# Kernel optimization log

Hardware: AMD Instinct MI355X
Metric: run time of the kernel (lower is better)

## Reference

```python
import jax, jax.numpy as jnp
import numpy as np

N_NODES = 50000
N_EDGES = 800000
N_IN = 96
N_HID = 96
N_CLS = 16
P_DROP = 0.5


def setup_inputs() -> dict:
    key = jax.random.key(0)
    ks = jax.random.split(key, 10)
    return {
        "features": jax.random.normal(ks[0], (N_NODES, N_IN), dtype=jnp.float32),
        "edge_weight": jax.random.uniform(ks[1], (N_EDGES,), dtype=jnp.float32),
        "src": jax.random.randint(ks[2], (N_EDGES,), 0, N_NODES),
        "dst": jax.random.randint(ks[3], (N_EDGES,), 0, N_NODES),
        "W0": jax.random.normal(ks[4], (N_IN, N_HID), dtype=jnp.float32) / np.sqrt(N_IN).astype(np.float32),
        "b0": jnp.zeros((N_HID,), dtype=jnp.float32),
        "W1": jax.random.normal(ks[5], (N_HID, N_HID), dtype=jnp.float32) / np.sqrt(N_HID).astype(np.float32),
        "b1": jnp.zeros((N_HID,), dtype=jnp.float32),
        "W2": jax.random.normal(ks[6], (N_HID, N_CLS), dtype=jnp.float32) / np.sqrt(N_HID).astype(np.float32),
        "b2": jnp.zeros((N_CLS,), dtype=jnp.float32),
    }


def reference(features, edge_weight, src, dst, W0, b0, W1, b1, W2, b2):
    N = features.shape[0]
    # Unweighted node degrees (DGL GraphConv norm='both'), clamped to >= 1.
    ones_e = jnp.ones_like(edge_weight)
    out_deg = jnp.clip(jax.ops.segment_sum(ones_e, src, num_segments=N), 1.0)
    in_deg = jnp.clip(jax.ops.segment_sum(ones_e, dst, num_segments=N), 1.0)
    inv_sqrt_out = out_deg ** -0.5  # [N]
    inv_sqrt_in = in_deg ** -0.5    # [N]

    def graph_conv(h, W, b, act):
        h = h * inv_sqrt_out[:, None]
        m = h[src] * edge_weight[:, None]                   # [E, d] gather + edge scale
        agg = jax.ops.segment_sum(m, dst, num_segments=N)   # [N, d] scatter-add
        out = (agg * inv_sqrt_in[:, None]) @ W + b          # D_in^-1/2, then linear + bias
        return act(out) if act is not None else out

    layers = [(W0, b0, jax.nn.relu), (W1, b1, jax.nn.relu), (W2, b2, None)]
    dkey = jax.random.key(42)
    h = features
    for i, (W, b, act) in enumerate(layers):
        keep = jax.random.bernoulli(jax.random.fold_in(dkey, i), 1.0 - P_DROP, h.shape)
        h = jnp.where(keep, h / (1.0 - P_DROP), 0.0)        # dropout p=0.5
        h = graph_conv(h, W, b, act)
    return jax.nn.log_softmax(h, axis=1)
```

## Files before the change

### kernel.cpp

```cpp
#include <hip/hip_runtime.h>
#include <hip/hip_fp16.h>
#include <stdint.h>

#define NNODES 50000
#define NEDGES 800000
#define NHID 96
#define NCLS 16

#define NC 100
#define NR 4
#define EPB (NEDGES / NC)
#define RNODES (NNODES / NR)
#define RWORDS8 (RNODES / 4)
#define NWORDS8 (NNODES / 4)
#define SCANB ((NWORDS8 + 255) / 256)
#define HISTBLKS (NC * NR)
#define FEPT8 8
#define FILLB3 ((NEDGES / FEPT8 + 255) / 256)
#define G96B ((NNODES + 127) / 128)
#define NDROP4 ((NNODES * NHID / 4 + 255) / 256)

__host__ __device__ inline void tf2x32(uint32_t k0, uint32_t k1, uint32_t x0, uint32_t x1,
                                       uint32_t& o0, uint32_t& o1) {
  uint32_t k2 = k0 ^ k1 ^ 0x1BD11BDAu;
#define TFROT(v, r) (((v) << (r)) | ((v) >> (32 - (r))))
#define TFR(r) { x0 += x1; x1 = TFROT(x1, r); x1 ^= x0; }
  x0 += k0; x1 += k1;
  TFR(13) TFR(15) TFR(26) TFR(6)
  x0 += k1; x1 += k2 + 1u;
  TFR(17) TFR(29) TFR(16) TFR(24)
  x0 += k2; x1 += k0 + 2u;
  TFR(13) TFR(15) TFR(26) TFR(6)
  x0 += k0; x1 += k1 + 3u;
  TFR(17) TFR(29) TFR(16) TFR(24)
  x0 += k1; x1 += k2 + 4u;
  TFR(13) TFR(15) TFR(26) TFR(6)
  x0 += k2; x1 += k0 + 5u;
  o0 = x0; o1 = x1;
#undef TFR
#undef TFROT
}

__device__ inline bool keep_bit(uint32_t k0, uint32_t k1, uint32_t j) {
  uint32_t o0, o1;
  tf2x32(k0, k1, 0u, j, o0, o1);
  return (((o0 ^ o1) >> 31) == 0u);
}

__global__ __launch_bounds__(256) void hist_drop_kernel(
    const int* __restrict__ src, const int* __restrict__ dst,
    uint32_t* __restrict__ slabD, uint32_t* __restrict__ slabS,
    uint8_t* __restrict__ rank8, uint32_t* __restrict__ flags,
    const float* __restrict__ h, float* __restrict__ X,
    uint32_t k0, uint32_t k1) {
  __shared__ uint32_t HD[RWORDS8];
  __shared__ uint32_t HS[RWORDS8];
  const int tid = threadIdx.x, b = blockIdx.x;
  if (b >= HISTBLKS) {
    int j = ((b - HISTBLKS) * 256 + tid) * 4;
    if (j < NNODES * NHID) {
      float4 hv = *(const float4*)(h + j);
      float4 o;
      o.x = keep_bit(k0, k1, (uint32_t)(j + 0)) ? hv.x * 2.0f : 0.0f;
      o.y = keep_bit(k0, k1, (uint32_t)(j + 1)) ? hv.y * 2.0f : 0.0f;
      o.z = keep_bit(k0, k1, (uint32_t)(j + 2)) ? hv.z * 2.0f : 0.0f;
      o.w = keep_bit(k0, k1, (uint32_t)(j + 3)) ? hv.w * 2.0f : 0.0f;
      *(float4*)(X + j) = o;
    }
    return;
  }
  if (b == 0 && tid < SCANB) flags[tid] = 0;
  const int c = b / NR, r = b - c * NR;
  const int e0 = c * EPB, e1 = e0 + EPB;
  const int nbase = r * RNODES;
  for (int w = tid; w < RWORDS8; w += 256) { HD[w] = 0; HS[w] = 0; }
  __syncthreads();
  int e = e0 + tid;
  for (; e + 768 < e1; e += 1024) {
    int d0 = dst[e] - nbase,       d1 = dst[e + 256] - nbase;
    int d2 = dst[e + 512] - nbase, d3 = dst[e + 768] - nbase;
    int s0 = src[e] - nbase,       s1 = src[e + 256] - nbase;
    int s2 = src[e + 512] - nbase, s3 = src[e + 768] - nbase;
    if ((unsigned)d0 < (unsigned)RNODES) {
      int sh = (d0 & 3) * 8;
      uint32_t old = atomicAdd(&HD[d0 >> 2], 1u << sh);
      rank8[e] = (uint8_t)((old >> sh) & 0xFFu);
    }
    if ((unsigned)d1 < (unsigned)RNODES) {
      int sh = (d1 & 3) * 8;
      uint32_t old = atomicAdd(&HD[d1 >> 2], 1u << sh);
      rank8[e + 256] = (uint8_t)((old >> sh) & 0xFFu);
    }
    if ((unsigned)d2 < (unsigned)RNODES) {
      int sh = (d2 & 3) * 8;
      uint32_t old = atomicAdd(&HD[d2 >> 2], 1u << sh);
      rank8[e + 512] = (uint8_t)((old >> sh) & 0xFFu);
    }
    if ((unsigned)d3 < (unsigned)RNODES) {
      int sh = (d3 & 3) * 8;
      uint32_t old = atomicAdd(&HD[d3 >> 2], 1u << sh);
      rank8[e + 768] = (uint8_t)((old >> sh) & 0xFFu);
    }
    if ((unsigned)s0 < (unsigned)RNODES) atomicAdd(&HS[s0 >> 2], 1u << ((s0 & 3) * 8));
    if ((unsigned)s1 < (unsigned)RNODES) atomicAdd(&HS[s1 >> 2], 1u << ((s1 & 3) * 8));
    if ((unsigned)s2 < (unsigned)RNODES) atomicAdd(&HS[s2 >> 2], 1u << ((s2 & 3) * 8));
    if ((unsigned)s3 < (unsigned)RNODES) atomicAdd(&HS[s3 >> 2], 1u << ((s3 & 3) * 8));
  }
  for (; e < e1; e += 256) {
    int d = dst[e] - nbase;
    if ((unsigned)d < (unsigned)RNODES) {
      int sh = (d & 3) * 8;
      uint32_t old = atomicAdd(&HD[d >> 2], 1u << sh);
      rank8[e] = (uint8_t)((old >> sh) & 0xFFu);
    }
    int s = src[e] - nbase;
    if ((unsigned)s < (unsigned)RNODES) atomicAdd(&HS[s >> 2], 1u << ((s & 3) * 8));
  }
  __syncthreads();
  uint32_t* dpD = slabD + (size_t)b * RWORDS8;
  uint32_t* dpS = slabS + (size_t)b * RWORDS8;
  for (int w = tid; w < RWORDS8; w += 256) { dpD[w] = HD[w]; dpS[w] = HS[w]; }
}

__global__ __launch_bounds__(256) void reduce_scan_kernel(
    const uint32_t* __restrict__ slabD, const uint32_t* __restrict__ slabS,
    float* __restrict__ inv_o, float* __restrict__ inv_i,
    uint32_t* __restrict__ rel8, int* __restrict__ row_ptr,
    uint32_t* __restrict__ flags) {
  __shared__ int lds[256];
  __shared__ int base_s;
  const int tid = threadIdx.x, b = blockIdx.x;
  const int gw = b * 256 + tid;
  uint32_t runD = 0, runS = 0;
  int n0 = 0;
  if (gw < NWORDS8) {
    int r = gw / RWORDS8, lw = gw - r * RWORDS8;
    n0 = r * RNODES + 4 * lw;
#pragma unroll 4
    for (int c = 0; c < NC; ++c) {
      rel8[(size_t)c * NWORDS8 + gw] = runD;
      runD += slabD[(size_t)(c * NR + r) * RWORDS8 + lw];
      runS += slabS[(size_t)(c * NR + r) * RWORDS8 + lw];
    }
  }
  const int d0 = runD & 0xFF, d1 = (runD >> 8) & 0xFF,
            d2 = (runD >> 16) & 0xFF, d3 = runD >> 24;
  const int tsum = d0 + d1 + d2 + d3;
  lds[tid] = tsum;
  __syncthreads();
  for (int off = 1; off < 256; off <<= 1) {
    int t = (tid >= off) ? lds[tid - off] : 0;
    __syncthreads();
    lds[tid] += t;
    __syncthreads();
  }
  const int incl = lds[tid];
  if (tid == 255) atomicExch(&flags[b], 0x80000000u | (uint32_t)lds[255]);
  if (tid < 64) {
    uint32_t part = 0;
    if (tid < b) {
      uint32_t v;
      do { v = atomicAdd(&flags[tid], 0u); } while (!(v & 0x80000000u));
      part = v & 0x7FFFFFFFu;
    }
#pragma unroll
    for (int off = 32; off > 0; off >>= 1)
      part += __shfl_down((unsigned)part, off, 64);
    if (tid == 0) base_s = (int)part;
  }
  __syncthreads();
  const int base = base_s;
  if (gw < NWORDS8) {
    int excl = base + incl - tsum;
    *(int4*)(row_ptr + n0) = make_int4(excl, excl + d0, excl + d0 + d1, excl + d0 + d1 + d2);
    *(float4*)(inv_i + n0) = make_float4(
        rsqrtf(fmaxf((float)d0, 1.0f)), rsqrtf(fmaxf((float)d1, 1.0f)),
        rsqrtf(fmaxf((float)d2, 1.0f)), rsqrtf(fmaxf((float)d3, 1.0f)));
    int o0 = runS & 0xFF, o1 = (runS >> 8) & 0xFF, o2 = (runS >> 16) & 0xFF, o3 = runS >> 24;
    *(float4*)(inv_o + n0) = make_float4(
        rsqrtf(fmaxf((float)o0, 1.0f)), rsqrtf(fmaxf((float)o1, 1.0f)),
        rsqrtf(fmaxf((float)o2, 1.0f)), rsqrtf(fmaxf((float)o3, 1.0f)));
    if (gw == NWORDS8 - 1) row_ptr[NNODES] = NEDGES;
  }
}

__global__ __launch_bounds__(256) void fill_gemm_kernel(
    const int* __restrict__ src, const int* __restrict__ dst, const float* __restrict__ ew,
    const uint8_t* __restrict__ rank8, const uint32_t* __restrict__ rel8,
    const int* __restrict__ row_ptr, const float* __restrict__ inv_o,
    uint32_t* __restrict__ csr,
    const float* __restrict__ X, const float* __restrict__ W, __half* __restrict__ Yh) {
  __shared__ float Wl[96 * 96];
  const int tid = threadIdx.x, b = blockIdx.x;
  if (b >= G96B) {
    int t = (b - G96B) * 256 + tid;
    int e = t * 8;
    if (e >= NEDGES) return;
    const uint32_t* rel = rel8 + (size_t)(e / EPB) * NWORDS8;
    int4 dA = *(const int4*)(dst + e), dB = *(const int4*)(dst + e + 4);
    int4 sA = *(const int4*)(src + e), sB = *(const int4*)(src + e + 4);
    float4 wA = *(const float4*)(ew + e), wB = *(const float4*)(ew + e + 4);
    uint2 r8 = *(const uint2*)(rank8 + e);
#pragma unroll
    for (int k = 0; k < 8; ++k) {
      int d = (k < 4) ? (&dA.x)[k] : (&dB.x)[k - 4];
      int s = (k < 4) ? (&sA.x)[k] : (&sB.x)[k - 4];
      float w = ((k < 4) ? (&wA.x)[k] : (&wB.x)[k - 4]) * inv_o[s];
      int rk = (int)(((k < 4 ? r8.x : r8.y) >> ((k & 3) * 8)) & 0xFFu);
      int sh = (d & 3) * 8;
      int rel_v = (int)((rel[d >> 2] >> sh) & 0xFFu);
      int pos = row_ptr[d] + rel_v + rk;
      uint32_t v = ((uint32_t)s << 16) | (uint32_t)__half_as_ushort(__float2half_rn(w));
      if ((unsigned)pos < (unsigned)NEDGES) csr[pos] = v;
    }
    return;
  }
  const int gb = b;
  {
    const float4* Wg = (const float4*)W;
    float4* Ws = (float4*)Wl;
#pragma unroll
    for (int i = 0; i < 9; ++i)
      Ws[tid + i * 256] = Wg[tid + i * 256];
  }
  __syncthreads();

  const int cg = tid & 7;
  const int rq = tid >> 3;
  const int row0 = gb * 128 + rq * 4;
  const int c0 = cg * 12;

  float acc[4][12];
#pragma unroll
  for (int r = 0; r < 4; ++r)
#pragma unroll
    for (int c = 0; c < 12; ++c) acc[r][c] = 0.f;

  const float* xr[4];
#pragma unroll
  for (int r = 0; r < 4; ++r) {
    int rr = row0 + r; if (rr > NNODES - 1) rr = NNODES - 1;
    xr[r] = X + (size_t)rr * 96;
  }

  for (int k = 0; k < 96; k += 4) {
    float4 x4[4];
#pragma unroll
    for (int r = 0; r < 4; ++r) x4[r] = *(const float4*)(xr[r] + k);
#pragma unroll
    for (int kk = 0; kk < 4; ++kk) {
      const float4* wp = (const float4*)(Wl + (k + kk) * 96 + c0);
      float4 w0 = wp[0], w1 = wp[1], w2 = wp[2];
      float xv[4] = { (&x4[0].x)[kk], (&x4[1].x)[kk], (&x4[2].x)[kk], (&x4[3].x)[kk] };
#pragma unroll
      for (int r = 0; r < 4; ++r) {
        acc[r][0]  += xv[r] * w0.x; acc[r][1]  += xv[r] * w0.y;
        acc[r][2]  += xv[r] * w0.z; acc[r][3]  += xv[r] * w0.w;
        acc[r][4]  += xv[r] * w1.x; acc[r][5]  += xv[r] * w1.y;
        acc[r][6]  += xv[r] * w1.z; acc[r][7]  += xv[r] * w1.w;
        acc[r][8]  += xv[r] * w2.x; acc[r][9]  += xv[r] * w2.y;
        acc[r][10] += xv[r] * w2.z; acc[r][11] += xv[r] * w2.w;
      }
    }
  }

#pragma unroll
  for (int r = 0; r < 4; ++r) {
    int rr = row0 + r;
    if (rr < NNODES) {
      __half2* hp = (__half2*)(Yh + (size_t)rr * 96 + c0);
#pragma unroll
      for (int c = 0; c < 6; ++c)
        hp[c] = __floats2half2_rn(acc[r][2 * c], acc[r][2 * c + 1]);
    }
  }
}

__global__ __launch_bounds__(256) void gemm96_kernel(
    const float* __restrict__ X, const float* __restrict__ W, __half* __restrict__ Yh) {
  __shared__ float Wl[96 * 96];
  const int tid = threadIdx.x;
  {
    const float4* Wg = (const float4*)W;
    float4* Ws = (float4*)Wl;
#pragma unroll
    for (int i = 0; i < 9; ++i)
      Ws[tid + i * 256] = Wg[tid + i * 256];
  }
  __syncthreads();

  const int cg = tid & 7;
  const int rq = tid >> 3;
  const int row0 = blockIdx.x * 128 + rq * 4;
  const int c0 = cg * 12;

  float acc[4][12];
#pragma unroll
  for (int r = 0; r < 4; ++r)
#pragma unroll
    for (int c = 0; c < 12; ++c) acc[r][c] = 0.f;

  const float* xr[4];
#pragma unroll
  for (int r = 0; r < 4; ++r) {
    int rr = row0 + r; if (rr > NNODES - 1) rr = NNODES - 1;
    xr[r] = X + (size_t)rr * 96;
  }

  for (int k = 0; k < 96; k += 4) {
    float4 x4[4];
#pragma unroll
    for (int r = 0; r < 4; ++r) x4[r] = *(const float4*)(xr[r] + k);
#pragma unroll
    for (int kk = 0; kk < 4; ++kk) {
      const float4* wp = (const float4*)(Wl + (k + kk) * 96 + c0);
      float4 w0 = wp[0], w1 = wp[1], w2 = wp[2];
      float xv[4] = { (&x4[0].x)[kk], (&x4[1].x)[kk], (&x4[2].x)[kk], (&x4[3].x)[kk] };
#pragma unroll
      for (int r = 0; r < 4; ++r) {
        acc[r][0]  += xv[r] * w0.x; acc[r][1]  += xv[r] * w0.y;
        acc[r][2]  += xv[r] * w0.z; acc[r][3]  += xv[r] * w0.w;
        acc[r][4]  += xv[r] * w1.x; acc[r][5]  += xv[r] * w1.y;
        acc[r][6]  += xv[r] * w1.z; acc[r][7]  += xv[r] * w1.w;
        acc[r][8]  += xv[r] * w2.x; acc[r][9]  += xv[r] * w2.y;
        acc[r][10] += xv[r] * w2.z; acc[r][11] += xv[r] * w2.w;
      }
    }
  }

#pragma unroll
  for (int r = 0; r < 4; ++r) {
    int rr = row0 + r;
    if (rr < NNODES) {
      __half2* hp = (__half2*)(Yh + (size_t)rr * 96 + c0);
#pragma unroll
      for (int c = 0; c < 6; ++c)
        hp[c] = __floats2half2_rn(acc[r][2 * c], acc[r][2 * c + 1]);
    }
  }
}

__global__ __launch_bounds__(256) void gemm16_kernel(
    const float* __restrict__ X, const float* __restrict__ W, __half* __restrict__ Y2h) {
  __shared__ float Wl[96 * 16];
  const int tid = threadIdx.x;
  {
    const float4* Wg = (const float4*)W;
    float4* Ws = (float4*)Wl;
    for (int i = tid; i < 384; i += 256) Ws[i] = Wg[i];
  }
  __syncthreads();

  const int row0 = blockIdx.x * 512 + tid * 2;
  const float* xr[2];
#pragma unroll
  for (int r = 0; r < 2; ++r) {
    int rr = row0 + r; if (rr > NNODES - 1) rr = NNODES - 1;
    xr[r] = X + (size_t)rr * 96;
  }

  float acc[2][16];
#pragma unroll
  for (int r = 0; r < 2; ++r)
#pragma unroll
    for (int c = 0; c < 16; ++c) acc[r][c] = 0.f;

  for (int k = 0; k < 96; k += 4) {
    float4 x4[2];
#pragma unroll
    for (int r = 0; r < 2; ++r) x4[r] = *(const float4*)(xr[r] + k);
#pragma unroll
    for (int kk = 0; kk < 4; ++kk) {
      const float4* wp = (const float4*)(Wl + (k + kk) * 16);
      float4 w0 = wp[0], w1 = wp[1], w2 = wp[2], w3 = wp[3];
#pragma unroll
      for (int r = 0; r < 2; ++r) {
        float xv = (&x4[r].x)[kk];
        acc[r][0]  += xv * w0.x; acc[r][1]  += xv * w0.y;
        acc[r][2]  += xv * w0.z; acc[r][3]  += xv * w0.w;
        acc[r][4]  += xv * w1.x; acc[r][5]  += xv * w1.y;
        acc[r][6]  += xv * w1.z; acc[r][7]  += xv * w1.w;
        acc[r][8]  += xv * w2.x; acc[r][9]  += xv * w2.y;
        acc[r][10] += xv * w2.z; acc[r][11] += xv * w2.w;
        acc[r][12] += xv * w3.x; acc[r][13] += xv * w3.y;
        acc[r][14] += xv * w3.z; acc[r][15] += xv * w3.w;
      }
    }
  }

#pragma unroll
  for (int r = 0; r < 2; ++r) {
    int rr = row0 + r;
    if (rr < NNODES) {
      __half2* hp = (__half2*)(Y2h + (size_t)rr * 16);
#pragma unroll
      for (int c = 0; c < 8; ++c)
        hp[c] = __floats2half2_rn(acc[r][2 * c], acc[r][2 * c + 1]);
    }
  }
}

#define ACC4(u0, wt) { \
  float2 g0 = __half22float2(*(__half2*)&u0.x); \
  float2 g1 = __half22float2(*(__half2*)&u0.y); \
  acc[0] += g0.x * wt; acc[1] += g0.y * wt; \
  acc[2] += g1.x * wt; acc[3] += g1.y * wt; }

__global__ __launch_bounds__(256) void gather96_drop_kernel(
    const __half* __restrict__ Yh, const uint32_t* __restrict__ csr,
    const int* __restrict__ row_ptr, const float* __restrict__ inv_in,
    const float* __restrict__ bias,
    float* __restrict__ Xn, uint32_t k0, uint32_t k1) {
  int tid = blockIdx.x * 256 + threadIdx.x;
  int n = tid / 24;
  int q = tid - n * 24;
  if (n >= NNODES) return;
  int beg = row_ptr[n], end = row_ptr[n + 1];
  float acc[4];
#pragma unroll
  for (int i = 0; i < 4; ++i) acc[i] = 0.f;

  int p = beg;
  for (; p + 8 <= end; p += 8) {
    uint32_t pw[8];
#pragma unroll
    for (int i = 0; i < 8; ++i) pw[i] = csr[p + i];
    float wv[8];
    uint2 u[8];
#pragma unroll
    for (int i = 0; i < 8; ++i) {
      int s = (int)(pw[i] >> 16); if (s >= NNODES) s = 0;
      wv[i] = __half2float(__ushort_as_half((unsigned short)(pw[i] & 0xFFFFu)));
      u[i] = *(const uint2*)(Yh + (size_t)s * 96 + q * 4);
    }
#pragma unroll
    for (int i = 0; i < 8; ++i) { ACC4(u[i], wv[i]) }
  }
  for (; p + 2 <= end; p += 2) {
    uint32_t pa = csr[p], pb = csr[p + 1];
    int s0 = pa >> 16, s1 = pb >> 16;
    if (s0 >= NNODES) s0 = 0;
    if (s1 >= NNODES) s1 = 0;
    float w0 = __half2float(__ushort_as_half((unsigned short)(pa & 0xFFFFu)));
    float w1 = __half2float(__ushort_as_half((unsigned short)(pb & 0xFFFFu)));
    uint2 a0 = *(const uint2*)(Yh + (size_t)s0 * 96 + q * 4);
    uint2 b0 = *(const uint2*)(Yh + (size_t)s1 * 96 + q * 4);
    ACC4(a0, w0)
    ACC4(b0, w1)
  }
  if (p < end) {
    uint32_t pa = csr[p];
    int s0 = pa >> 16;
    if (s0 >= NNODES) s0 = 0;
    float w0 = __half2float(__ushort_as_half((unsigned short)(pa & 0xFFFFu)));
    uint2 a0 = *(const uint2*)(Yh + (size_t)s0 * 96 + q * 4);
    ACC4(a0, w0)
  }

  float iv = inv_in[n];
  const float* bp = bias + q * 4;
  float o[4];
#pragma unroll
  for (int i = 0; i < 4; ++i)
    o[i] = fmaxf(acc[i] * iv + bp[i], 0.f) * 2.0f;
  uint32_t jb = (uint32_t)(n * 96 + q * 4);
#pragma unroll
  for (int i = 0; i < 4; ++i)
    o[i] = keep_bit(k0, k1, jb + i) ? o[i] : 0.f;
  float* xp = Xn + (size_t)n * 96 + q * 4;
  *(float4*)xp = make_float4(o[0], o[1], o[2], o[3]);
}

__global__ __launch_bounds__(256) void gather16_lsm_kernel(
    const __half* __restrict__ Y2h, const uint32_t* __restrict__ csr,
    const int* __restrict__ row_ptr, const float* __restrict__ inv_in,
    const float* __restrict__ b2, float* __restrict__ out) {
  int t = blockIdx.x * 256 + threadIdx.x;
  int n = t >> 2;
  int q = t & 3;
  if (n >= NNODES) return;
  int beg = row_ptr[n], end = row_ptr[n + 1];
  float acc[4];
#pragma unroll
  for (int i = 0; i < 4; ++i) acc[i] = 0.f;

  int p = beg;
  for (; p + 4 <= end; p += 4) {
    uint32_t pa = csr[p], pb = csr[p + 1], pc = csr[p + 2], pd = csr[p + 3];
    int sa = pa >> 16, sb = pb >> 16, sc_ = pc >> 16, sd = pd >> 16;
    if (sa >= NNODES) sa = 0;
    if (sb >= NNODES) sb = 0;
    if (sc_ >= NNODES) sc_ = 0;
    if (sd >= NNODES) sd = 0;
    float wa = __half2float(__ushort_as_half((unsigned short)(pa & 0xFFFFu)));
    float wb = __half2float(__ushort_as_half((unsigned short)(pb & 0xFFFFu)));
    float wc = __half2float(__ushort_as_half((unsigned short)(pc & 0xFFFFu)));
    float wd = __half2float(__ushort_as_half((unsigned short)(pd & 0xFFFFu)));
    uint2 a0 = *(const uint2*)(Y2h + (size_t)sa * 16 + q * 4);
    uint2 b0 = *(const uint2*)(Y2h + (size_t)sb * 16 + q * 4);
    uint2 c0 = *(const uint2*)(Y2h + (size_t)sc_ * 16 + q * 4);
    uint2 d0 = *(const uint2*)(Y2h + (size_t)sd * 16 + q * 4);
    ACC4(a0, wa) ACC4(b0, wb) ACC4(c0, wc) ACC4(d0, wd)
  }
  for (; p + 2 <= end; p += 2) {
    uint32_t pa = csr[p], pb = csr[p + 1];
    int sa = pa >> 16, sb = pb >> 16;
    if (sa >= NNODES) sa = 0;
    if (sb >= NNODES) sb = 0;
    float wa = __half2float(__ushort_as_half((unsigned short)(pa & 0xFFFFu)));
    float wb = __half2float(__ushort_as_half((unsigned short)(pb & 0xFFFFu)));
    uint2 a0 = *(const uint2*)(Y2h + (size_t)sa * 16 + q * 4);
    uint2 b0 = *(const uint2*)(Y2h + (size_t)sb * 16 + q * 4);
    ACC4(a0, wa) ACC4(b0, wb)
  }
  if (p < end) {
    uint32_t pa = csr[p];
    int sa = pa >> 16;
    if (sa >= NNODES) sa = 0;
    float wa = __half2float(__ushort_as_half((unsigned short)(pa & 0xFFFFu)));
    uint2 a0 = *(const uint2*)(Y2h + (size_t)sa * 16 + q * 4);
    ACC4(a0, wa)
  }

  float iv = inv_in[n];
  float v[4];
#pragma unroll
  for (int i = 0; i < 4; ++i) v[i] = acc[i] * iv + b2[q * 4 + i];
  float m = v[0];
#pragma unroll
  for (int i = 1; i < 4; i++) m = fmaxf(m, v[i]);
  m = fmaxf(m, __shfl_xor(m, 1));
  m = fmaxf(m, __shfl_xor(m, 2));
  float s = 0.f;
#pragma unroll
  for (int i = 0; i < 4; i++) s += expf(v[i] - m);
  s += __shfl_xor(s, 1);
  s += __shfl_xor(s, 2);
  float ls = logf(s);
  float* orow = out + (size_t)n * 16 + q * 4;
  *(float4*)orow = make_float4(v[0] - m - ls, v[1] - m - ls, v[2] - m - ls, v[3] - m - ls);
}

extern "C" void kernel_launch(void* const* d_in, const int* in_sizes, int n_in,
                              void* d_out, int out_size, void* d_ws, size_t ws_size,
                              hipStream_t stream) {
  const float* feat = (const float*)d_in[0];
  const float* ew   = (const float*)d_in[1];
  const int*   src  = (const int*)d_in[2];
  const int*   dst  = (const int*)d_in[3];
  const float* W0   = (const float*)d_in[4];
  const float* b0   = (const float*)d_in[5];
  const float* W1   = (const float*)d_in[6];
  const float* b1   = (const float*)d_in[7];
  const float* W2   = (const float*)d_in[8];
  const float* b2   = (const float*)d_in[9];
  float* out = (float*)d_out;

  char* base = (char*)d_ws;
  size_t off = 0;
  auto take = [&](size_t nbytes) {
    void* q = base + off;
    off += (nbytes + 255) & ~(size_t)255;
    return q;
  };
  uint32_t* flags   = (uint32_t*)take((size_t)SCANB * 4);
  int*      row_ptr = (int*)take((size_t)(NNODES + 1) * 4);
  float*    inv_o   = (float*)take((size_t)NNODES * 4);
  float*    inv_i   = (float*)take((size_t)NNODES * 4);
  uint32_t* slabD   = (uint32_t*)take((size_t)NC * NR * RWORDS8 * 4);
  uint32_t* slabS   = (uint32_t*)take((size_t)NC * NR * RWORDS8 * 4);
  uint32_t* rel8    = (uint32_t*)take((size_t)NC * NWORDS8 * 4);
  uint8_t*  rank8   = (uint8_t*)take((size_t)NEDGES);
  uint32_t* csr     = (uint32_t*)take((size_t)NEDGES * 4);
  float*    X       = (float*)take((size_t)NNODES * NHID * 4);
  __half*   Yh      = (__half*)take((size_t)NNODES * NHID * 2);
  __half*   Y2h     = (__half*)take((size_t)NNODES * NCLS * 2);
  (void)ws_size; (void)in_sizes; (void)n_in; (void)out_size;

  uint32_t k[3][2];
  for (uint32_t i = 0; i < 3; i++) tf2x32(0u, 42u, 0u, i, k[i][0], k[i][1]);

  hist_drop_kernel<<<HISTBLKS + NDROP4, 256, 0, stream>>>(
      src, dst, slabD, slabS, rank8, flags, feat, X, k[0][0], k[0][1]);
  reduce_scan_kernel<<<SCANB, 256, 0, stream>>>(slabD, slabS, inv_o, inv_i, rel8, row_ptr, flags);
  fill_gemm_kernel<<<G96B + FILLB3, 256, 0, stream>>>(
      src, dst, ew, rank8, rel8, row_ptr, inv_o, csr, X, W0, Yh);

  const int G16  = (NNODES + 511) / 512;
  const int GGD  = (NNODES * 24 + 255) / 256;
  const int GLSM = (NNODES * 4 + 255) / 256;

  gather96_drop_kernel<<<GGD, 256, 0, stream>>>(Yh, csr, row_ptr, inv_i, b0, X, k[1][0], k[1][1]);
  gemm96_kernel<<<G96B, 256, 0, stream>>>(X, W1, Yh);
  gather96_drop_kernel<<<GGD, 256, 0, stream>>>(Yh, csr, row_ptr, inv_i, b1, X, k[2][0], k[2][1]);
  gemm16_kernel<<<G16, 256, 0, stream>>>(X, W2, Y2h);
  gather16_lsm_kernel<<<GLSM, 256, 0, stream>>>(Y2h, csr, row_ptr, inv_i, b2, out);
}
```

Before: 249.5 us.

## Partition CSR fill blocks by edge chunk and destination node range

The CSR fill part of the fused fill/GEMM kernel now gives each block one edge chunk and one eighth of the destination node range. Each block scans all edges in its chunk and writes only those whose destination falls in its range. The aim is to keep the scattered csr writes and the row_ptr/rel8 lookups inside a narrow address window, for better cache locality. In exchange every dst index is read eight times, and the per-thread work drops from vectorised 8-edge loads to a strided loop. The GEMM block count is also padded by one, which relies on the GEMM path guarding out-of-range rows.

```diff
diff --git a/kernel.cpp b/kernel.cpp
--- a/kernel.cpp
+++ b/kernel.cpp
@@ -15,9 +15,11 @@
 #define NWORDS8 (NNODES / 4)
 #define SCANB ((NWORDS8 + 255) / 256)
 #define HISTBLKS (NC * NR)
-#define FEPT8 8
-#define FILLB3 ((NEDGES / FEPT8 + 255) / 256)
 #define G96B ((NNODES + 127) / 128)
+#define G96PAD 392
+#define FR 8
+#define FRNODES (NNODES / FR)
+#define FILLB4 (NC * FR)
 #define NDROP4 ((NNODES * NHID / 4 + 255) / 256)
 
 __host__ __device__ inline void tf2x32(uint32_t k0, uint32_t k1, uint32_t x0, uint32_t x1,
@@ -192,26 +194,25 @@
     const float* __restrict__ X, const float* __restrict__ W, __half* __restrict__ Yh) {
   __shared__ float Wl[96 * 96];
   const int tid = threadIdx.x, b = blockIdx.x;
-  if (b >= G96B) {
-    int t = (b - G96B) * 256 + tid;
-    int e = t * 8;
-    if (e >= NEDGES) return;
-    const uint32_t* rel = rel8 + (size_t)(e / EPB) * NWORDS8;
-    int4 dA = *(const int4*)(dst + e), dB = *(const int4*)(dst + e + 4);
-    int4 sA = *(const int4*)(src + e), sB = *(const int4*)(src + e + 4);
-    float4 wA = *(const float4*)(ew + e), wB = *(const float4*)(ew + e + 4);
-    uint2 r8 = *(const uint2*)(rank8 + e);
-#pragma unroll
-    for (int k = 0; k < 8; ++k) {
-      int d = (k < 4) ? (&dA.x)[k] : (&dB.x)[k - 4];
-      int s = (k < 4) ? (&sA.x)[k] : (&sB.x)[k - 4];
-      float w = ((k < 4) ? (&wA.x)[k] : (&wB.x)[k - 4]) * inv_o[s];
-      int rk = (int)(((k < 4 ? r8.x : r8.y) >> ((k & 3) * 8)) & 0xFFu);
-      int sh = (d & 3) * 8;
-      int rel_v = (int)((rel[d >> 2] >> sh) & 0xFFu);
-      int pos = row_ptr[d] + rel_v + rk;
-      uint32_t v = ((uint32_t)s << 16) | (uint32_t)__half_as_ushort(__float2half_rn(w));
-      if ((unsigned)pos < (unsigned)NEDGES) csr[pos] = v;
+  if (b >= G96PAD) {
+    const int i = b - G96PAD;
+    const int r = i & 7;
+    const int c = i >> 3;
+    const int e0 = c * EPB, e1 = e0 + EPB;
+    const int lo = r * FRNODES, hi = lo + FRNODES;
+    const uint32_t* rel = rel8 + (size_t)c * NWORDS8;
+    for (int e = e0 + tid; e < e1; e += 256) {
+      int d = dst[e];
+      if (d >= lo && d < hi) {
+        int s = src[e];
+        float w = ew[e] * inv_o[s];
+        int rk = (int)rank8[e];
+        int sh = (d & 3) * 8;
+        int rel_v = (int)((rel[d >> 2] >> sh) & 0xFFu);
+        int pos = row_ptr[d] + rel_v + rk;
+        uint32_t v = ((uint32_t)s << 16) | (uint32_t)__half_as_ushort(__float2half_rn(w));
+        if ((unsigned)pos < (unsigned)NEDGES) csr[pos] = v;
+      }
     }
     return;
   }
@@ -583,7 +584,7 @@
   hist_drop_kernel<<<HISTBLKS + NDROP4, 256, 0, stream>>>(
       src, dst, slabD, slabS, rank8, flags, feat, X, k[0][0], k[0][1]);
   reduce_scan_kernel<<<SCANB, 256, 0, stream>>>(slabD, slabS, inv_o, inv_i, rel8, row_ptr, flags);
-  fill_gemm_kernel<<<G96B + FILLB3, 256, 0, stream>>>(
+  fill_gemm_kernel<<<G96PAD + FILLB4, 256, 0, stream>>>(
       src, dst, ew, rank8, rel8, row_ptr, inv_o, csr, X, W0, Yh);
 
   const int G16  = (NNODES + 511) / 512;
```

Result: slower. 267.9 us (+7.4%).
